# Performance work log

Hardware: AMD Instinct MI355X
Metric: run time of the kernel (lower is better)

## Reference

```python
import jax, jax.numpy as jnp
import numpy as np

B, IN_F, OUT_F, GRID = 8192, 1024, 1024, 5


def setup_inputs() -> dict:
    key = jax.random.key(0)
    k1, k2, k3, k4 = jax.random.split(key, 4)
    X = jax.random.normal(k1, (B, IN_F), dtype=jnp.float32)
    # Per-edge linear B-spline coefficients on a uniform grid over [-1, 1]
    coeffs = jax.random.normal(k2, (OUT_F, GRID), dtype=jnp.float32) * 0.1
    # Per-edge 2->1 Linear (PyTorch default init: U(-s, s), s = 1/sqrt(fan_in=2))
    s = 1.0 / np.sqrt(2.0)
    W = jax.random.uniform(k3, (OUT_F, 2), dtype=jnp.float32, minval=-s, maxval=s)
    b = jax.random.uniform(k4, (OUT_F,), dtype=jnp.float32, minval=-s, maxval=s)
    return {"X": X, "coeffs": coeffs, "W": W, "b": b}


def _bspline_linear(x, coeffs):
    # x: [B, O], coeffs: [O, G]. Linear (degree-1) B-spline interpolation on
    # a uniform knot grid over [-1, 1]; x clamped to the grid range.
    G = coeffs.shape[1]
    h = 2.0 / (G - 1)                      # knot spacing
    t = (jnp.clip(x, -1.0, 1.0) + 1.0) / h  # grid coordinate in [0, G-1]
    k = jnp.clip(jnp.floor(t), 0, G - 2).astype(jnp.int32)  # left knot index
    frac = t - k
    e = jnp.arange(coeffs.shape[0])[None, :]  # per-edge row index [1, O]
    c0 = coeffs[e, k]
    c1 = coeffs[e, k + 1]
    return c0 * (1.0 - frac) + c1 * frac


def reference(X, coeffs, W, b):
    # X: [B, in_f]; coeffs: [O, G]; W: [O, 2]; b: [O]  ->  Y: [B, O]
    in_f = X.shape[1]
    O = W.shape[0]
    idx_in = jnp.arange(O) % in_f          # edge i reads input i % in_features
    x = X[:, idx_in]                        # [B, O]
    silu = jax.nn.silu(x)                   # [B, O]
    spline = _bspline_linear(x, coeffs)     # [B, O]
    # Per-edge 2->1 linear combine: Y[:, i] = W[i,0]*silu + W[i,1]*spline + b[i]
    Y = silu * W[:, 0][None, :] + spline * W[:, 1][None, :] + b[None, :]
    return Y
```

## Files before the change

### kernel.cpp

```cpp
#include <hip/hip_runtime.h>
#include <math.h>


#define B_ROWS   8192
#define N_FEAT   1024
#define N_BLOCKS 2048
#define ROWS_PER_BLOCK (B_ROWS / N_BLOCKS)

__global__ __launch_bounds__(256) void kan_kernel(
    const float* __restrict__ X,
    const float* __restrict__ coeffs,
    const float* __restrict__ W,
    const float* __restrict__ bias,
    float* __restrict__ Y)
{
    const int t    = threadIdx.x;
    const int col0 = t * 4;

    float c0[4], d0[4], d1[4], d2[4], d3[4], w0[4], w1[4], bb[4];
#pragma unroll
    for (int j = 0; j < 4; ++j) {
        const int col = col0 + j;
        const float* cp = coeffs + col * 5;
        const float a0 = cp[0], a1 = cp[1], a2 = cp[2], a3 = cp[3], a4 = cp[4];
        c0[j] = a0;
        d0[j] = a1 - a0;
        d1[j] = a2 - a1;
        d2[j] = a3 - a2;
        d3[j] = a4 - a3;
        w0[j] = W[col * 2 + 0];
        w1[j] = W[col * 2 + 1];
        bb[j] = bias[col];
    }

#pragma unroll
    for (int i = 0; i < ROWS_PER_BLOCK; ++i) {
        const int row = blockIdx.x + i * N_BLOCKS;
        const size_t base = (size_t)row * N_FEAT + col0;

        const float4 x4 = *reinterpret_cast<const float4*>(X + base);
        const float xs[4] = {x4.x, x4.y, x4.z, x4.w};
        float ys[4];

#pragma unroll
        for (int j = 0; j < 4; ++j) {
            const float x = xs[j];

            const float sig  = 1.0f / (1.0f + __expf(-x));
            const float silu = x * sig;

            const float xc = fminf(fmaxf(x, -1.0f), 1.0f);
            const float tt = fmaf(2.0f, xc, 2.0f);
            const float r0 = fminf(tt, 1.0f);
            const float r1 = fminf(fmaxf(tt - 1.0f, 0.0f), 1.0f);
            const float r2 = fminf(fmaxf(tt - 2.0f, 0.0f), 1.0f);
            const float r3 = fminf(fmaxf(tt - 3.0f, 0.0f), 1.0f);
            float s = c0[j];
            s = fmaf(d0[j], r0, s);
            s = fmaf(d1[j], r1, s);
            s = fmaf(d2[j], r2, s);
            s = fmaf(d3[j], r3, s);

            ys[j] = fmaf(silu, w0[j], fmaf(s, w1[j], bb[j]));
        }

        *reinterpret_cast<float4*>(Y + base) =
            make_float4(ys[0], ys[1], ys[2], ys[3]);
    }
}

extern "C" void kernel_launch(void* const* d_in, const int* in_sizes, int n_in,
                              void* d_out, int out_size, void* d_ws, size_t ws_size,
                              hipStream_t stream) {
    const float* X      = (const float*)d_in[0];
    const float* coeffs = (const float*)d_in[1];
    const float* W      = (const float*)d_in[2];
    const float* b      = (const float*)d_in[3];
    float* Y            = (float*)d_out;

    kan_kernel<<<N_BLOCKS, 256, 0, stream>>>(X, coeffs, W, b, Y);
}
```

Before: 88.42 us.

## Vectorize parameter loads, halve block count, batch row loads up front

```diff
diff --git a/kernel.cpp b/kernel.cpp
--- a/kernel.cpp
+++ b/kernel.cpp
@@ -4,7 +4,7 @@
 
 #define B_ROWS   8192
 #define N_FEAT   1024
-#define N_BLOCKS 2048
+#define N_BLOCKS 1024
 #define ROWS_PER_BLOCK (B_ROWS / N_BLOCKS)
 
 __global__ __launch_bounds__(256) void kan_kernel(
@@ -17,29 +17,47 @@
     const int t    = threadIdx.x;
     const int col0 = t * 4;
 
-    float c0[4], d0[4], d1[4], d2[4], d3[4], w0[4], w1[4], bb[4];
+    float craw[20];
+    {
+        const float4* cg = reinterpret_cast<const float4*>(coeffs + (size_t)col0 * 5);
+        float4* cr = reinterpret_cast<float4*>(craw);
+#pragma unroll
+        for (int q = 0; q < 5; ++q) cr[q] = cg[q];
+    }
+    float wraw[8];
+    {
+        const float4* wg = reinterpret_cast<const float4*>(W + (size_t)col0 * 2);
+        float4* wr = reinterpret_cast<float4*>(wraw);
+        wr[0] = wg[0]; wr[1] = wg[1];
+    }
+    const float4 b4 = *reinterpret_cast<const float4*>(bias + col0);
+    const float bb[4] = {b4.x, b4.y, b4.z, b4.w};
+
+    float c0[4], d0[4], d1[4], d2[4], d3[4], w0[4], w1[4];
 #pragma unroll
     for (int j = 0; j < 4; ++j) {
-        const int col = col0 + j;
-        const float* cp = coeffs + col * 5;
-        const float a0 = cp[0], a1 = cp[1], a2 = cp[2], a3 = cp[3], a4 = cp[4];
+        const float a0 = craw[j * 5 + 0], a1 = craw[j * 5 + 1], a2 = craw[j * 5 + 2];
+        const float a3 = craw[j * 5 + 3], a4 = craw[j * 5 + 4];
         c0[j] = a0;
         d0[j] = a1 - a0;
         d1[j] = a2 - a1;
         d2[j] = a3 - a2;
         d3[j] = a4 - a3;
-        w0[j] = W[col * 2 + 0];
-        w1[j] = W[col * 2 + 1];
-        bb[j] = bias[col];
+        w0[j] = wraw[j * 2 + 0];
+        w1[j] = wraw[j * 2 + 1];
+    }
+
+    float4 x4[ROWS_PER_BLOCK];
+#pragma unroll
+    for (int i = 0; i < ROWS_PER_BLOCK; ++i) {
+        const int row = blockIdx.x + i * N_BLOCKS;
+        x4[i] = *reinterpret_cast<const float4*>(X + (size_t)row * N_FEAT + col0);
     }
 
 #pragma unroll
     for (int i = 0; i < ROWS_PER_BLOCK; ++i) {
         const int row = blockIdx.x + i * N_BLOCKS;
-        const size_t base = (size_t)row * N_FEAT + col0;
-
-        const float4 x4 = *reinterpret_cast<const float4*>(X + base);
-        const float xs[4] = {x4.x, x4.y, x4.z, x4.w};
+        const float xs[4] = {x4[i].x, x4[i].y, x4[i].z, x4[i].w};
         float ys[4];
 
 #pragma unroll
@@ -55,8 +73,7 @@
             const float r1 = fminf(fmaxf(tt - 1.0f, 0.0f), 1.0f);
             const float r2 = fminf(fmaxf(tt - 2.0f, 0.0f), 1.0f);
             const float r3 = fminf(fmaxf(tt - 3.0f, 0.0f), 1.0f);
-            float s = c0[j];
-            s = fmaf(d0[j], r0, s);
+            float s = fmaf(d0[j], r0, c0[j]);
             s = fmaf(d1[j], r1, s);
             s = fmaf(d2[j], r2, s);
             s = fmaf(d3[j], r3, s);
@@ -64,7 +81,7 @@
             ys[j] = fmaf(silu, w0[j], fmaf(s, w1[j], bb[j]));
         }
 
-        *reinterpret_cast<float4*>(Y + base) =
+        *reinterpret_cast<float4*>(Y + (size_t)row * N_FEAT + col0) =
             make_float4(ys[0], ys[1], ys[2], ys[3]);
     }
 }
```

Result: no change. 88.95 us (+0.6%).
